# Kernel tuning notes

Hardware: AMD Instinct MI355X
Metric: run time of the kernel (lower is better)

Reference implementation:

```python
import jax, jax.numpy as jnp
import numpy as np

E = 1024      # embed_dim
H = 16        # num_heads
HD = E // H   # head_dim = 64
WIN = 256     # window_size
LN_EPS = 1e-5


def _layernorm(x, g, b):
    mu = jnp.mean(x, axis=-1, keepdims=True)
    var = jnp.var(x, axis=-1, keepdims=True)
    return (x - mu) * jax.lax.rsqrt(var + LN_EPS) * g + b


def _rope_tables(S):
    freqs = 1.0 / (10000.0 ** (jnp.arange(0, HD, 2, dtype=jnp.float32) / HD))  # [HD/2]
    t = jnp.arange(S, dtype=jnp.float32)
    fr = jnp.outer(t, freqs)                      # [S, HD/2]
    emb = jnp.concatenate([fr, fr], axis=-1)      # [S, HD]
    # shape [S, 1, HD] so it broadcasts over the heads dim of [B, S, H, HD]
    return emb[:, None, :].astype(jnp.float32), None


def _rotate_half(x):
    x1, x2 = jnp.split(x, 2, axis=-1)
    return jnp.concatenate([-x2, x1], axis=-1)


def setup_inputs() -> dict:
    key = jax.random.key(0)
    ks = jax.random.split(key, 12)
    B, S = 8, 1024
    sc = 0.02
    return {
        "x": jax.random.normal(ks[0], (B, S, E), dtype=jnp.float32),
        "in_proj_w": jax.random.normal(ks[1], (3 * E, E), dtype=jnp.float32) * sc,
        "in_proj_b": jnp.zeros((3 * E,), dtype=jnp.float32),
        "out_proj_w": jax.random.normal(ks[2], (E, E), dtype=jnp.float32) * sc,
        "out_proj_b": jnp.zeros((E,), dtype=jnp.float32),
        "ln1_g": jnp.ones((E,), dtype=jnp.float32),
        "ln1_b": jnp.zeros((E,), dtype=jnp.float32),
        "w1": jax.random.normal(ks[3], (4 * E, E), dtype=jnp.float32) * sc,
        "b1": jnp.zeros((4 * E,), dtype=jnp.float32),
        "w2": jax.random.normal(ks[4], (E, 4 * E), dtype=jnp.float32) * sc,
        "b2": jnp.zeros((E,), dtype=jnp.float32),
        "ln2_g": jnp.ones((E,), dtype=jnp.float32),
        "ln2_b": jnp.zeros((E,), dtype=jnp.float32),
    }


def reference(x, in_proj_w, in_proj_b, out_proj_w, out_proj_b,
              ln1_g, ln1_b, w1, b1, w2, b2, ln2_g, ln2_b):
    B, S, _ = x.shape
    # RoPE applied to the raw input (pre in_proj), as in the torch module
    emb, _ = _rope_tables(S)
    cos, sin = jnp.cos(emb), jnp.sin(emb)          # [S, 1, HD]
    xh = x.reshape(B, S, H, HD)
    roped = xh * cos + _rotate_half(xh) * sin      # [B, S, H, HD]
    qk_in = roped.reshape(B, S, E)

    Wq, Wk, Wv = jnp.split(in_proj_w, 3, axis=0)   # each [E, E]
    bq, bk, bv = jnp.split(in_proj_b, 3, axis=0)
    q = (qk_in @ Wq.T + bq).reshape(B, S, H, HD).transpose(0, 2, 1, 3)  # [B,H,S,HD]
    k = (qk_in @ Wk.T + bk).reshape(B, S, H, HD).transpose(0, 2, 1, 3)
    v = (x @ Wv.T + bv).reshape(B, S, H, HD).transpose(0, 2, 1, 3)

    scale = 1.0 / np.sqrt(HD)
    scores = jnp.einsum("bhqd,bhkd->bhqk", q, k) * scale  # [B,H,S,S]
    idx = jnp.arange(S)
    disallowed = jnp.abs(idx[:, None] - idx[None, :]) > WIN  # [S,S] bool
    scores = jnp.where(disallowed, jnp.float32(-jnp.inf), scores)
    attn = jax.nn.softmax(scores, axis=-1)
    ctx = jnp.einsum("bhqk,bhkd->bhqd", attn, v)            # [B,H,S,HD]
    ctx = ctx.transpose(0, 2, 1, 3).reshape(B, S, E)
    h = ctx @ out_proj_w.T + out_proj_b

    x1 = _layernorm(x + h, ln1_g, ln1_b)
    ff = jax.nn.gelu(x1 @ w1.T + b1, approximate=False) @ w2.T + b2
    return _layernorm(x1 + ff, ln2_g, ln2_b)
```

## Files before the change

### kernel.cpp

```cpp
#include <hip/hip_runtime.h>
#include <stdint.h>


#define B_ 8
#define S_ 1024
#define E_ 1024
#define H_ 16
#define HD_ 64
#define WIN_ 256
#define QKV_ 3072

typedef __attribute__((ext_vector_type(8))) short short8;
typedef __attribute__((ext_vector_type(4))) float f32x4;
typedef __attribute__((ext_vector_type(4))) unsigned short us4;
typedef unsigned short ushort_t;

__device__ __forceinline__ ushort_t f2b(float f) {
  unsigned int u = __builtin_bit_cast(unsigned int, f);
  u = (u + 0x7fffu + ((u >> 16) & 1u)) >> 16;
  return (ushort_t)u;
}

__device__ __forceinline__ ushort_t f2b_trunc(float f) {
  return (ushort_t)(__builtin_bit_cast(unsigned int, f) >> 16);
}

__device__ __forceinline__ float b2f(ushort_t u) {
  return __builtin_bit_cast(float, ((unsigned int)u) << 16);
}

__device__ __forceinline__ float fast_exp2(float x) {
#if __has_builtin(__builtin_amdgcn_exp2f)
  return __builtin_amdgcn_exp2f(x);
#else
  return exp2f(x);
#endif
}

__device__ __forceinline__ float fast_rcp(float x) {
#if __has_builtin(__builtin_amdgcn_rcpf)
  return __builtin_amdgcn_rcpf(x);
#else
  return 1.f / x;
#endif
}

__device__ __forceinline__ void gld_lds16(const void* g, void* l) {
  __builtin_amdgcn_global_load_lds((const __attribute__((address_space(1))) void*)g,
                                   (__attribute__((address_space(3))) void*)l, 16, 0, 0);
}

__global__ __launch_bounds__(256) void cast4_kernel(const float* __restrict__ i0,
                                                    const float* __restrict__ i1,
                                                    const float* __restrict__ i2,
                                                    const float* __restrict__ i3,
                                                    ushort_t* __restrict__ o0,
                                                    ushort_t* __restrict__ o1,
                                                    ushort_t* __restrict__ o2,
                                                    ushort_t* __restrict__ o3) {
  int i = blockIdx.x * 256 + threadIdx.x;
  const float* in;
  ushort_t* out;
  int j;
  if (i < 786432)       { in = i0; out = o0; j = i; }
  else if (i < 1048576) { in = i1; out = o1; j = i - 786432; }
  else if (i < 2097152) { in = i2; out = o2; j = i - 1048576; }
  else                  { in = i3; out = o3; j = i - 2097152; }
  float4 v = ((const float4*)in)[j];
  us4 o;
  o.x = f2b(v.x); o.y = f2b(v.y); o.z = f2b(v.z); o.w = f2b(v.w);
  ((us4*)out)[j] = o;
}

__global__ __launch_bounds__(256) void rope_kernel(const float* __restrict__ x,
                                                   ushort_t* __restrict__ roped,
                                                   ushort_t* __restrict__ xbf) {
  int idx = blockIdx.x * 256 + threadIdx.x;
  int d = idx & 31;
  int h = (idx >> 5) & 15;
  int s = (idx >> 9) & 1023;
  int b = idx >> 19;
  size_t base = ((size_t)(b * S_ + s)) * E_ + h * HD_ + d;
  float x0 = x[base], x1 = x[base + 32];
  float freq = exp2f(-(float)d * 0.41524101186092029f);
  float th = (float)s * freq;
  float sn, cs;
  sincosf(th, &sn, &cs);
  roped[base]      = f2b(x0 * cs - x1 * sn);
  roped[base + 32] = f2b(x1 * cs + x0 * sn);
  xbf[base]      = f2b(x0);
  xbf[base + 32] = f2b(x1);
}

template <int MODE>
__global__ __launch_bounds__(256) void gemm_bt(const ushort_t* __restrict__ A,
                                               const ushort_t* __restrict__ A2,
                                               int nsplit,
                                               const ushort_t* __restrict__ Bm,
                                               const float* __restrict__ bias,
                                               ushort_t* __restrict__ C,
                                               int N, int K) {
  __shared__ ushort_t sA[128 * 64];
  __shared__ ushort_t sB[128 * 64];
  const int tid = threadIdx.x;
  const int lane = tid & 63;
  const int wave = tid >> 6;
  const int quad = lane >> 4;
  const int lq = lane & 15;
  const int wm = (wave & 1) * 64;
  const int wn = (wave >> 1) * 64;
  const size_t bm = (size_t)blockIdx.x * 128;
  const size_t bn = (size_t)blockIdx.y * 128;
  const ushort_t* Asel = (bn >= (size_t)nsplit) ? A2 : A;

  f32x4 acc[4][4] = {};

  const int srow = lane >> 3;
  const int skc = ((lane & 7) ^ (lane >> 3)) * 8;

  for (int k0 = 0; k0 < K; k0 += 64) {
#pragma unroll
    for (int i = 0; i < 4; i++) {
      const int r0 = wave * 32 + i * 8;
      gld_lds16(Asel + (bm + r0 + srow) * K + k0 + skc, &sA[r0 * 64]);
      gld_lds16(Bm + (bn + r0 + srow) * K + k0 + skc, &sB[r0 * 64]);
    }
    __syncthreads();

#pragma unroll
    for (int kk = 0; kk < 2; kk++) {
      const int csw = (((kk * 4) + quad) ^ (lq & 7)) * 8;
      short8 av[4], bv[4];
#pragma unroll
      for (int mt = 0; mt < 4; mt++)
        av[mt] = *(const short8*)&sA[(wm + mt * 16 + lq) * 64 + csw];
#pragma unroll
      for (int nt = 0; nt < 4; nt++)
        bv[nt] = *(const short8*)&sB[(wn + nt * 16 + lq) * 64 + csw];
#pragma unroll
      for (int mt = 0; mt < 4; mt++)
#pragma unroll
        for (int nt = 0; nt < 4; nt++)
          acc[mt][nt] = __builtin_amdgcn_mfma_f32_16x16x32_bf16(av[mt], bv[nt], acc[mt][nt], 0, 0, 0);
    }
    __syncthreads();
  }

#pragma unroll
  for (int mt = 0; mt < 4; mt++) {
#pragma unroll
    for (int nt = 0; nt < 4; nt++) {
      size_t row = bm + wm + mt * 16 + quad * 4;
      size_t col = bn + wn + nt * 16 + lq;
      float bc = bias[col];
#pragma unroll
      for (int r = 0; r < 4; r++) {
        float v = acc[mt][nt][r] + bc;
        if (MODE == 1) {
          float y = 0.7978845608028654f * (v + 0.044715f * v * v * v);
          float t = fast_exp2(y * 2.8853900817779268f);
          v = v * (t * fast_rcp(1.f + t));
        }
        C[(row + r) * N + col] = f2b(v);
      }
    }
  }
}

__global__ __launch_bounds__(256) void vtrans_kernel(const ushort_t* __restrict__ qkv,
                                                     ushort_t* __restrict__ vt) {
  __shared__ ushort_t tb[64 * 65];
  int bh = blockIdx.x >> 4;
  int st = blockIdx.x & 15;
  int b = bh >> 4, h = bh & 15;
  int s0 = st * 64;
  int tid = threadIdx.x;
  int c = tid & 63, rbase = tid >> 6;
#pragma unroll
  for (int rep = 0; rep < 16; rep++) {
    int i = rep * 4 + rbase;
    tb[c * 65 + i] = qkv[(size_t)(b * S_ + s0 + i) * QKV_ + 2048 + h * HD_ + c];
  }
  __syncthreads();
#pragma unroll
  for (int rep = 0; rep < 16; rep++) {
    int d = rep * 4 + rbase;
    vt[(size_t)((b * H_ + h) * HD_ + d) * S_ + s0 + c] = tb[d * 65 + c];
  }
}

#define SC_ 0.18033688011112042f

__global__ __launch_bounds__(256) void attn_kernel(const ushort_t* __restrict__ qkv,
                                                   const ushort_t* __restrict__ vt,
                                                   ushort_t* __restrict__ ctx) {
  __shared__ ushort_t sK[2][32 * 64];
  __shared__ ushort_t sV[2][64 * 32];
  __shared__ ushort_t sP[4][16 * 36];
  const int tid = threadIdx.x;
  const int lane = tid & 63, wave = tid >> 6;
  const int quad = lane >> 4, lq = lane & 15;
  int gid = ((blockIdx.x & 7) << 8) | (blockIdx.x >> 3);
  int qs = gid & 15;
  int h = (gid >> 4) & 15;
  int b = gid >> 8;
  int qs64 = qs * 64;
  int q0 = qs64 + wave * 16;

  const size_t qoff = (size_t)(b * S_ + q0 + lq) * QKV_ + h * HD_;
  short8 a0 = *(const short8*)&qkv[qoff + quad * 8];
  short8 a1 = *(const short8*)&qkv[qoff + 32 + quad * 8];

  f32x4 o[4] = {};
  float rs[4] = {0.f, 0.f, 0.f, 0.f};

  int start = qs64 - WIN_; if (start < 0) start = 0;
  int end = qs64 + 64 + WIN_; if (end > S_) end = S_;
  const int wlo = q0 - WIN_;
  const int whi = q0 + 16 + WIN_;

  const ushort_t* kg = qkv + (size_t)(b * S_) * QKV_ + 1024 + h * HD_;
  const ushort_t* vg = vt + (size_t)((b * H_ + h) * HD_) * S_;

  const int krow = lane >> 3;
  const int kchg = ((lane & 7) ^ krow) << 3;
  const int vrow = lane >> 2;
  const int vchg = ((lane & 3) ^ ((lane >> 3) & 3)) << 3;

  gld_lds16(kg + (size_t)(start + wave * 8 + krow) * QKV_ + kchg, &sK[0][wave * 512]);
  gld_lds16(vg + (size_t)(wave * 16 + vrow) * S_ + start + vchg, &sV[0][wave * 512]);

  const int nch = (end - start) >> 5;
  int buf = 0;
  for (int c = 0; c < nch; c++) {
    __syncthreads();
    int kb = start + c * 32;
    if (c + 1 < nch) {
      int nkb = kb + 32;
      gld_lds16(kg + (size_t)(nkb + wave * 8 + krow) * QKV_ + kchg, &sK[buf ^ 1][wave * 512]);
      gld_lds16(vg + (size_t)(wave * 16 + vrow) * S_ + nkb + vchg, &sV[buf ^ 1][wave * 512]);
    }
    if (kb < whi && kb + 32 > wlo) {
      f32x4 s[2];
#pragma unroll
      for (int t = 0; t < 2; t++) {
        const ushort_t* kr = &sK[buf][(t * 16 + lq) * 64];
        short8 b0 = *(const short8*)&kr[((quad ^ (lq & 7)) << 3)];
        short8 b1 = *(const short8*)&kr[(((4 + quad) ^ (lq & 7)) << 3)];
        f32x4 z = {};
        z = __builtin_amdgcn_mfma_f32_16x16x32_bf16(a0, b0, z, 0, 0, 0);
        z = __builtin_amdgcn_mfma_f32_16x16x32_bf16(a1, b1, z, 0, 0, 0);
        s[t] = z;
      }
      float p[2][4];
      const bool full = (kb >= q0 - 241) && (kb <= q0 + 225);
      if (full) {
#pragma unroll
        for (int t = 0; t < 2; t++)
#pragma unroll
          for (int r = 0; r < 4; r++) p[t][r] = fast_exp2(s[t][r] * SC_);
      } else {
#pragma unroll
        for (int t = 0; t < 2; t++) {
          int ki = kb + t * 16 + lq;
#pragma unroll
          for (int r = 0; r < 4; r++) {
            int dd = q0 + quad * 4 + r - ki;
            bool allowed = (dd <= WIN_) && (dd >= -WIN_);
            p[t][r] = allowed ? fast_exp2(s[t][r] * SC_) : 0.f;
          }
        }
      }
#pragma unroll
      for (int r = 0; r < 4; r++) rs[r] += p[0][r] + p[1][r];

#pragma unroll
      for (int t = 0; t < 2; t++)
#pragma unroll
        for (int r = 0; r < 4; r++)
          sP[wave][(quad * 4 + r) * 36 + t * 16 + lq] = f2b_trunc(p[t][r]);
      asm volatile("s_waitcnt lgkmcnt(0)" ::: "memory");
      short8 ap = *(const short8*)&sP[wave][lq * 36 + quad * 8];

#pragma unroll
      for (int nt = 0; nt < 4; nt++) {
        short8 bvf = *(const short8*)&sV[buf][(nt * 16 + lq) * 32 +
                                             ((quad ^ ((lq >> 1) & 3)) << 3)];
        o[nt] = __builtin_amdgcn_mfma_f32_16x16x32_bf16(ap, bvf, o[nt], 0, 0, 0);
      }
    }
    buf ^= 1;
  }

  float inv[4];
#pragma unroll
  for (int r = 0; r < 4; r++) {
    float v = rs[r];
    v += __shfl_xor(v, 1);
    v += __shfl_xor(v, 2);
    v += __shfl_xor(v, 4);
    v += __shfl_xor(v, 8);
    inv[r] = 1.f / v;
  }

#pragma unroll
  for (int nt = 0; nt < 4; nt++)
#pragma unroll
    for (int r = 0; r < 4; r++) {
      int row = q0 + quad * 4 + r;
      int col = h * HD_ + nt * 16 + lq;
      ctx[(size_t)(b * S_ + row) * E_ + col] = f2b(o[nt][r] * inv[r]);
    }
}

__global__ __launch_bounds__(256) void ln_res_kernel(const float* __restrict__ A,
                                                     const ushort_t* __restrict__ Bv,
                                                     const float* __restrict__ g,
                                                     const float* __restrict__ be,
                                                     float* __restrict__ outf,
                                                     ushort_t* __restrict__ outb) {
  const int row = blockIdx.x;
  const int tid = threadIdx.x;
  const size_t base = (size_t)row * 1024;
  float4 a4 = ((const float4*)(A + base))[tid];
  us4 b4 = ((const us4*)(Bv + base))[tid];
  float v[4];
  v[0] = a4.x + b2f(b4.x);
  v[1] = a4.y + b2f(b4.y);
  v[2] = a4.z + b2f(b4.z);
  v[3] = a4.w + b2f(b4.w);
  float s = v[0] + v[1] + v[2] + v[3];
  float sq = v[0] * v[0] + v[1] * v[1] + v[2] * v[2] + v[3] * v[3];
#pragma unroll
  for (int off = 32; off; off >>= 1) {
    s += __shfl_xor(s, off);
    sq += __shfl_xor(sq, off);
  }
  __shared__ float ls[4], lsq[4];
  int wave = tid >> 6, lane = tid & 63;
  if (lane == 0) { ls[wave] = s; lsq[wave] = sq; }
  __syncthreads();
  s = ls[0] + ls[1] + ls[2] + ls[3];
  sq = lsq[0] + lsq[1] + lsq[2] + lsq[3];
  float mean = s * (1.f / 1024.f);
  float var = sq * (1.f / 1024.f) - mean * mean;
  float rstd = rsqrtf(var + 1e-5f);
  float4 g4 = ((const float4*)g)[tid];
  float4 e4 = ((const float4*)be)[tid];
  float o0 = (v[0] - mean) * rstd * g4.x + e4.x;
  float o1 = (v[1] - mean) * rstd * g4.y + e4.y;
  float o2 = (v[2] - mean) * rstd * g4.z + e4.z;
  float o3 = (v[3] - mean) * rstd * g4.w + e4.w;
  float4 of = {o0, o1, o2, o3};
  ((float4*)(outf + base))[tid] = of;
  if (outb) {
    us4 ob;
    ob.x = f2b(o0); ob.y = f2b(o1); ob.z = f2b(o2); ob.w = f2b(o3);
    ((us4*)(outb + base))[tid] = ob;
  }
}

#define O_XBF   ((size_t)0)
#define O_ROPED ((size_t)16777216)
#define O_W_IN  ((size_t)33554432)
#define O_W_OUT ((size_t)39845888)
#define O_W1    ((size_t)41943040)
#define O_W2    ((size_t)50331648)
#define O_BIG   ((size_t)58720256)
#define O_VT    ((size_t)125829120)
#define O_X1F   ((size_t)142606336)
#define O_FF2   ((size_t)176160768)

extern "C" void kernel_launch(void* const* d_in, const int* in_sizes, int n_in,
                              void* d_out, int out_size, void* d_ws, size_t ws_size,
                              hipStream_t stream) {
  const float* x          = (const float*)d_in[0];
  const float* in_proj_w  = (const float*)d_in[1];
  const float* in_proj_b  = (const float*)d_in[2];
  const float* out_proj_w = (const float*)d_in[3];
  const float* out_proj_b = (const float*)d_in[4];
  const float* ln1_g      = (const float*)d_in[5];
  const float* ln1_b      = (const float*)d_in[6];
  const float* w1         = (const float*)d_in[7];
  const float* b1         = (const float*)d_in[8];
  const float* w2         = (const float*)d_in[9];
  const float* b2         = (const float*)d_in[10];
  const float* ln2_g      = (const float*)d_in[11];
  const float* ln2_b      = (const float*)d_in[12];
  float* out = (float*)d_out;

  char* ws = (char*)d_ws;
  ushort_t* xbf     = (ushort_t*)(ws + O_XBF);
  ushort_t* roped   = (ushort_t*)(ws + O_ROPED);
  ushort_t* wbf_in  = (ushort_t*)(ws + O_W_IN);
  ushort_t* wbf_out = (ushort_t*)(ws + O_W_OUT);
  ushort_t* wbf_1   = (ushort_t*)(ws + O_W1);
  ushort_t* wbf_2   = (ushort_t*)(ws + O_W2);
  ushort_t* qkv_buf = (ushort_t*)(ws + O_BIG);
  ushort_t* vtb     = (ushort_t*)(ws + O_VT);
  ushort_t* ctx     = (ushort_t*)(ws + O_ROPED);
  ushort_t* h_bf    = (ushort_t*)(ws + O_BIG);
  float*    x1f     = (float*)(ws + O_X1F);
  ushort_t* x1bf    = (ushort_t*)(ws + O_XBF);
  ushort_t* ff1     = (ushort_t*)(ws + O_BIG);
  ushort_t* ff2     = (ushort_t*)(ws + O_FF2);

  dim3 blk(256);
  const int NOSPLIT = 1 << 30;

  cast4_kernel<<<dim3(12288), blk, 0, stream>>>(in_proj_w, out_proj_w, w1, w2,
                                                wbf_in, wbf_out, wbf_1, wbf_2);

  rope_kernel<<<dim3(16384), blk, 0, stream>>>(x, roped, xbf);

  gemm_bt<0><<<dim3(64, 24), blk, 0, stream>>>(roped, xbf, 2048, wbf_in, in_proj_b,
                                               qkv_buf, QKV_, 1024);
  vtrans_kernel<<<dim3(2048), blk, 0, stream>>>(qkv_buf, vtb);

  attn_kernel<<<dim3(2048), blk, 0, stream>>>(qkv_buf, vtb, ctx);

  gemm_bt<0><<<dim3(64, 8), blk, 0, stream>>>(ctx, ctx, NOSPLIT, wbf_out, out_proj_b,
                                              h_bf, 1024, 1024);

  ln_res_kernel<<<dim3(8192), blk, 0, stream>>>(x, h_bf, ln1_g, ln1_b, x1f, x1bf);

  gemm_bt<1><<<dim3(64, 32), blk, 0, stream>>>(x1bf, x1bf, NOSPLIT, wbf_1, b1,
                                               ff1, 4096, 1024);

  gemm_bt<0><<<dim3(64, 8), blk, 0, stream>>>(ff1, ff1, NOSPLIT, wbf_2, b2,
                                              ff2, 1024, 4096);

  ln_res_kernel<<<dim3(8192), blk, 0, stream>>>(x1f, ff2, ln2_g, ln2_b, out, nullptr);
}
```

Before: 480.3 us.

## Add 256x256-tile 8-wave pipelined GEMM for QKV and FFN1 projections

```diff
diff --git a/kernel.cpp b/kernel.cpp
--- a/kernel.cpp
+++ b/kernel.cpp
@@ -162,6 +162,142 @@
           v = v * (t * fast_rcp(1.f + t));
         }
         C[(row + r) * N + col] = f2b(v);
+      }
+    }
+  }
+}
+
+#define FENCE asm volatile("" ::: "memory")
+#define VM4 asm volatile("s_waitcnt vmcnt(4)" ::: "memory")
+#define VM0 asm volatile("s_waitcnt vmcnt(0)" ::: "memory")
+#define NOPW ((void)0)
+
+#define STAGE_A(bufc, half, kb)                                               \
+  { gld_lds16(aSrc + (size_t)((half) * 128) * K + (kb),                       \
+              &lds[16384 * (bufc) + 8192 * (half) + wave * 512]);             \
+    gld_lds16(aSrc + (size_t)((half) * 128 + 64) * K + (kb),                  \
+              &lds[16384 * (bufc) + 8192 * (half) + 4096 + wave * 512]); }
+
+#define STAGE_B(bufc, half, kb)                                               \
+  { gld_lds16(bSrc + (size_t)((half) * 128) * K + (kb),                       \
+              &lds[32768 + 16384 * (bufc) + 8192 * (half) + wave * 512]);     \
+    gld_lds16(bSrc + (size_t)((half) * 128 + 64) * K + (kb),                  \
+              &lds[32768 + 16384 * (bufc) + 8192 * (half) + 4096 + wave * 512]); }
+
+#define PHASE(qq, bufc, doA, doB, STAGE_STMT, WAIT_STMT)                      \
+  {                                                                           \
+    if (doA) {                                                                \
+      const int abase = 16384 * (bufc) + 8192 * ((qq) >> 1);                  \
+      _Pragma("unroll") for (int mf = 0; mf < 4; mf++) {                      \
+        const int ra = wm * 64 + mf * 16 + lq;                                \
+        _Pragma("unroll") for (int k2 = 0; k2 < 2; k2++)                      \
+          av[mf][k2] = *(const short8*)&lds[abase + ra * 64 +                 \
+                                            (((k2 * 4 + quad) ^ (lq & 7)) << 3)]; \
+      }                                                                       \
+    }                                                                         \
+    if (doB) {                                                                \
+      const int bbase = 32768 + 16384 * (bufc) +                              \
+                        8192 * ((((qq) == 1) || ((qq) == 2)) ? 1 : 0);        \
+      _Pragma("unroll") for (int nf = 0; nf < 2; nf++) {                      \
+        const int rb = wn * 32 + nf * 16 + lq;                                \
+        _Pragma("unroll") for (int k2 = 0; k2 < 2; k2++)                      \
+          bv[nf][k2] = *(const short8*)&lds[bbase + rb * 64 +                 \
+                                            (((k2 * 4 + quad) ^ (lq & 7)) << 3)]; \
+      }                                                                       \
+    }                                                                         \
+    STAGE_STMT;                                                               \
+    FENCE; __builtin_amdgcn_s_barrier(); FENCE;                               \
+    __builtin_amdgcn_s_setprio(1);                                            \
+    _Pragma("unroll") for (int k2 = 0; k2 < 2; k2++)                          \
+      _Pragma("unroll") for (int mf = 0; mf < 4; mf++)                        \
+        _Pragma("unroll") for (int nf = 0; nf < 2; nf++)                      \
+          acc[qq][mf][nf] = __builtin_amdgcn_mfma_f32_16x16x32_bf16(          \
+              av[mf][k2], bv[nf][k2], acc[qq][mf][nf], 0, 0, 0);              \
+    __builtin_amdgcn_s_setprio(0);                                            \
+    WAIT_STMT;                                                                \
+    FENCE; __builtin_amdgcn_s_barrier(); FENCE;                               \
+  }
+
+template <int MODE>
+__global__ __launch_bounds__(512, 2) void gemm256(const ushort_t* __restrict__ A,
+                                                  const ushort_t* __restrict__ A2,
+                                                  int nsplit,
+                                                  const ushort_t* __restrict__ Bm,
+                                                  const float* __restrict__ bias,
+                                                  ushort_t* __restrict__ C,
+                                                  int N, int K, int nbx) {
+  __shared__ ushort_t lds[65536];
+  const int tid = threadIdx.x;
+  const int lane = tid & 63, wave = tid >> 6;
+  const int quad = lane >> 4, lq = lane & 15;
+  const int wm = wave >> 2, wn = wave & 3;
+
+  const int nwg = gridDim.x;
+  const int id = blockIdx.x;
+  const int wg = (nwg & 7) ? id : ((id & 7) * (nwg >> 3) + (id >> 3));
+  const int bx = wg % nbx, by = wg / nbx;
+  const size_t bm = (size_t)bx * 256, bn = (size_t)by * 256;
+  const ushort_t* Asel = ((int)bn >= nsplit) ? A2 : A;
+
+  const int srow = lane >> 3;
+  const int scol = ((lane & 7) ^ srow) << 3;
+  const ushort_t* aSrc = Asel + (bm + wave * 8 + srow) * (size_t)K + scol;
+  const ushort_t* bSrc = Bm + (bn + wave * 8 + srow) * (size_t)K + scol;
+
+  f32x4 acc[4][4][2] = {};
+  short8 av[4][2], bv[2][2];
+
+  STAGE_A(0, 0, 0); STAGE_A(0, 1, 0); STAGE_B(0, 0, 0); STAGE_B(0, 1, 0);
+  STAGE_A(1, 0, 64); STAGE_B(1, 1, 64);
+  VM4;
+  FENCE; __builtin_amdgcn_s_barrier(); FENCE;
+
+  const int NT = K >> 6;
+#pragma unroll 1
+  for (int i = 0; i < (NT >> 1) - 1; i++) {
+    const int kb0 = i << 7;
+    PHASE(0, 0, 1, 1, STAGE_A(1, 1, kb0 + 64), NOPW);
+    PHASE(1, 0, 0, 1, STAGE_B(1, 0, kb0 + 64), NOPW);
+    PHASE(2, 0, 1, 0, STAGE_A(0, 0, kb0 + 128), NOPW);
+    PHASE(3, 0, 0, 1, STAGE_B(0, 1, kb0 + 128), VM4);
+    PHASE(0, 1, 1, 1, STAGE_A(0, 1, kb0 + 128), NOPW);
+    PHASE(1, 1, 0, 1, STAGE_B(0, 0, kb0 + 128), NOPW);
+    PHASE(2, 1, 1, 0, STAGE_A(1, 0, kb0 + 192), NOPW);
+    PHASE(3, 1, 0, 1, STAGE_B(1, 1, kb0 + 192), VM4);
+  }
+  {
+    const int kb0 = (NT - 2) << 6;
+    PHASE(0, 0, 1, 1, STAGE_A(1, 1, kb0 + 64), NOPW);
+    PHASE(1, 0, 0, 1, STAGE_B(1, 0, kb0 + 64), NOPW);
+    PHASE(2, 0, 1, 0, NOPW, NOPW);
+    PHASE(3, 0, 0, 1, NOPW, VM0);
+    PHASE(0, 1, 1, 1, NOPW, NOPW);
+    PHASE(1, 1, 0, 1, NOPW, NOPW);
+    PHASE(2, 1, 1, 0, NOPW, NOPW);
+    PHASE(3, 1, 0, 1, NOPW, NOPW);
+  }
+
+#pragma unroll
+  for (int q = 0; q < 4; q++) {
+    const int Mh = q >> 1;
+    const int Nh = (q == 1 || q == 2) ? 1 : 0;
+#pragma unroll
+    for (int mf = 0; mf < 4; mf++) {
+#pragma unroll
+      for (int nf = 0; nf < 2; nf++) {
+        size_t row = bm + Mh * 128 + wm * 64 + mf * 16 + quad * 4;
+        size_t col = bn + Nh * 128 + wn * 32 + nf * 16 + lq;
+        float bc = bias[col];
+#pragma unroll
+        for (int r = 0; r < 4; r++) {
+          float v = acc[q][mf][nf][r] + bc;
+          if (MODE == 1) {
+            float y = 0.7978845608028654f * (v + 0.044715f * v * v * v);
+            float t = fast_exp2(y * 2.8853900817779268f);
+            v = v * (t * fast_rcp(1.f + t));
+          }
+          C[(row + r) * N + col] = f2b(v);
+        }
       }
     }
   }
@@ -406,6 +542,7 @@
   ushort_t* ff2     = (ushort_t*)(ws + O_FF2);
 
   dim3 blk(256);
+  dim3 blk512(512);
   const int NOSPLIT = 1 << 30;
 
   cast4_kernel<<<dim3(12288), blk, 0, stream>>>(in_proj_w, out_proj_w, w1, w2,
@@ -413,8 +550,8 @@
 
   rope_kernel<<<dim3(16384), blk, 0, stream>>>(x, roped, xbf);
 
-  gemm_bt<0><<<dim3(64, 24), blk, 0, stream>>>(roped, xbf, 2048, wbf_in, in_proj_b,
-                                               qkv_buf, QKV_, 1024);
+  gemm256<0><<<dim3(384), blk512, 0, stream>>>(roped, xbf, 2048, wbf_in, in_proj_b,
+                                               qkv_buf, QKV_, 1024, 32);
   vtrans_kernel<<<dim3(2048), blk, 0, stream>>>(qkv_buf, vtb);
 
   attn_kernel<<<dim3(2048), blk, 0, stream>>>(qkv_buf, vtb, ctx);
@@ -424,8 +561,8 @@
 
   ln_res_kernel<<<dim3(8192), blk, 0, stream>>>(x, h_bf, ln1_g, ln1_b, x1f, x1bf);
 
-  gemm_bt<1><<<dim3(64, 32), blk, 0, stream>>>(x1bf, x1bf, NOSPLIT, wbf_1, b1,
-                                               ff1, 4096, 1024);
+  gemm256<1><<<dim3(512), blk512, 0, stream>>>(x1bf, x1bf, NOSPLIT, wbf_1, b1,
+                                               ff1, 4096, 1024, 32);
 
   gemm_bt<0><<<dim3(64, 8), blk, 0, stream>>>(ff1, ff1, NOSPLIT, wbf_2, b2,
                                               ff2, 1024, 4096);
```

Result: faster. 466.1 us (-3.0%).
